# Kernel optimization log

Hardware: AMD Instinct MI355X
Metric: run time of the kernel (lower is better)

Reference implementation:

```python
import jax, jax.numpy as jnp
import numpy as np

N = 128       # n_channels
B = 131072    # batch
C = np.float32(np.sqrt(0.5))  # 50/50 beamsplitter amplitude (c = s = sqrt(0.5))


def setup_inputs() -> dict:
    key = jax.random.key(0)
    k1, k2, k3, k4 = jax.random.split(key, 4)
    M = N * (N - 1) // 2
    return {
        "x_real": jax.random.normal(k1, (B, N), jnp.float32),
        "x_imag": jax.random.normal(k2, (B, N), jnp.float32),
        "mzi_phases": jax.random.normal(k3, (M * 2,), jnp.float32) * 0.1,
        "output_phases": jax.random.normal(k4, (N,), jnp.float32) * 0.1,
    }


def _construct_unitary(mzi_phases, output_phases):
    n = output_phases.shape[0]
    m = n * (n - 1) // 2
    # pair ordering matches the torch double loop: i ascending, then j > i (row-major triu)
    i_np, j_np = np.triu_indices(n, 1)
    i_idx = jnp.asarray(i_np, jnp.int32)
    j_idx = jnp.asarray(j_np, jnp.int32)
    ph = mzi_phases.reshape(m, 2)
    theta, phi = ph[:, 0], ph[:, 1]

    def step(U, xs):
        th, ph_, i, j = xs
        e_phi = jax.lax.complex(jnp.cos(ph_), jnp.sin(ph_))
        e_th = jax.lax.complex(jnp.cos(th), jnp.sin(th))
        ri = U[i]
        rj = U[j]
        # T_ij @ U touches only rows i and j (O(N) Givens row update)
        new_i = C * ri + (C * e_phi) * rj
        new_j = (C * e_th) * ri - (C * e_th * e_phi) * rj
        U = U.at[i].set(new_i).at[j].set(new_j)
        return U, None

    def chunk_body(U, xs_chunk):
        U, _ = jax.lax.scan(step, U, xs_chunk)
        return U, None

    # chunk the M sequential updates: M = (n-1) * (n//2) for even n;
    # checkpointing chunks keeps reverse-mode memory O(sqrt-ish) instead of O(M * N^2)
    n_chunks = n - 1
    cs = n // 2
    xs = (theta.reshape(n_chunks, cs), phi.reshape(n_chunks, cs),
          i_idx.reshape(n_chunks, cs), j_idx.reshape(n_chunks, cs))
    U0 = jnp.eye(n, dtype=jnp.complex64)
    U, _ = jax.lax.scan(jax.checkpoint(chunk_body), U0, xs)
    # output phase screen D @ U
    d = jax.lax.complex(jnp.cos(output_phases), jnp.sin(output_phases))
    return d[:, None] * U


def reference(x_real, x_imag, mzi_phases, output_phases):
    U = _construct_unitary(mzi_phases, output_phases)           # [N, N] complex64
    x = jax.lax.complex(x_real, x_imag)                          # [B, N] complex64
    # matmul(U, x.unsqueeze(-1)).squeeze(-1) == x @ U^T
    out = jnp.einsum('nm,bm->bn', U, x)                          # [B, N] complex64
    # ComplexDropout is identity in eval mode
    return out
```

## Files before the change

kernel.cpp:

```cpp
#include <hip/hip_runtime.h>
#include <hip/hip_bf16.h>

#define NDIM 128
#define N2   (NDIM * NDIM)
#define BDIM 131072
#define NMZI 8128
#define NCHUNK 8
#define NBLK 32
#define NJG 8
#define NCOL 32
#define NLOC 16
static constexpr float CC = 0.70710678118654752440f;

typedef __attribute__((ext_vector_type(8))) short bf16x8;
typedef __attribute__((ext_vector_type(4))) float f32x4;

__device__ __align__(16) float2         g_V[NCHUNK * N2];
__device__ __align__(16) float2         g_W[4 * N2];
__device__ __align__(16) float2         g_Y[2 * N2];
__device__ __align__(16) unsigned short g_TB[32 * NDIM * 8];
__device__ __align__(16) unsigned short g_Ur[16 * NDIM * 8];
__device__ __align__(16) unsigned short g_Ui[16 * NDIM * 8];
__device__ unsigned g_ctr[3];

__device__ inline unsigned short f2bf(float f) {
    union { __hip_bfloat16 h; unsigned short u; } cv;
    cv.h = __float2bfloat16(f);
    return cv.u;
}

__device__ __forceinline__ void gbar(int idx) {
    __syncthreads();
    asm volatile("" ::: "memory");
    if (threadIdx.x == 0) {
        __threadfence();
        __hip_atomic_fetch_add(&g_ctr[idx], 1u, __ATOMIC_ACQ_REL, __HIP_MEMORY_SCOPE_AGENT);
        while (__hip_atomic_load(&g_ctr[idx], __ATOMIC_ACQUIRE, __HIP_MEMORY_SCOPE_AGENT)
               < (unsigned)NBLK)
            __builtin_amdgcn_s_sleep(8);
        __threadfence();
    }
    __syncthreads();
    asm volatile("" ::: "memory");
}

#define CFMA(acc, av, b)                                                    \
    acc.x = fmaf(av.x, b.x, fmaf(-av.y, b.y, acc.x));                       \
    acc.y = fmaf(av.x, b.y, fmaf( av.y, b.x, acc.y));

template <int MODE>
__device__ __forceinline__ void compose_unit(const float2* __restrict__ A,
                                             const float2* __restrict__ B,
                                             float2* __restrict__ Cout,
                                             const float* __restrict__ oph,
                                             int n0, int m, float2* __restrict__ As,
                                             bool active) {
    __syncthreads();
    if (active) {
        #pragma unroll
        for (int r = 0; r < 4; ++r) As[r * NDIM + m] = A[(n0 + r) * NDIM + m];
    }
    __syncthreads();
    if (!active) return;

    float2 a0 = {0.f, 0.f}, a1 = {0.f, 0.f}, a2 = {0.f, 0.f}, a3 = {0.f, 0.f};
    float2 bb[8];
    #pragma unroll
    for (int u = 0; u < 8; ++u) bb[u] = B[u * NDIM + m];

    #pragma unroll 1
    for (int k0 = 0; k0 < NDIM; k0 += 8) {
        #pragma unroll
        for (int u = 0; u < 8; ++u) {
            const float2 b = bb[u];
            bb[u] = B[(k0 + 8 + u) * NDIM + m];
            const int k = k0 + u;
            float2 v;
            v = As[0 * NDIM + k]; CFMA(a0, v, b)
            v = As[1 * NDIM + k]; CFMA(a1, v, b)
            v = As[2 * NDIM + k]; CFMA(a2, v, b)
            v = As[3 * NDIM + k]; CFMA(a3, v, b)
        }
    }
    if (MODE == 0) {
        Cout[(n0 + 0) * NDIM + m] = a0;
        Cout[(n0 + 1) * NDIM + m] = a1;
        Cout[(n0 + 2) * NDIM + m] = a2;
        Cout[(n0 + 3) * NDIM + m] = a3;
    } else {
        const int kg = m >> 3, e = m & 7;
        #pragma unroll
        for (int r = 0; r < 4; ++r) {
            const int n = n0 + r;
            const float2 u = (r == 0) ? a0 : (r == 1) ? a1 : (r == 2) ? a2 : a3;
            float ds, dc;
            sincosf(oph[n], &ds, &dc);
            const float vr = fmaf(u.x, dc, -u.y * ds);
            const float vi = fmaf(u.x, ds,  u.y * dc);
            g_TB[(kg * NDIM + n) * 8 + e]        = f2bf(vr);
            g_TB[((16 + kg) * NDIM + n) * 8 + e] = f2bf(-vi);
            g_Ur[(kg * NDIM + n) * 8 + e] = f2bf(vr);
            g_Ui[(kg * NDIM + n) * 8 + e] = f2bf(vi);
        }
    }
}

__global__ __launch_bounds__(256) void build_all(const float* __restrict__ mzi,
                                                 const float* __restrict__ oph) {
    __shared__ __align__(16) char SM[40960];
    const int tid = threadIdx.x;
    const int b   = blockIdx.x;

    {
        float2 (*Usm)[NCOL] = reinterpret_cast<float2(*)[NCOL]>(SM);
        float4 (*ph)[NDIM]  = reinterpret_cast<float4(*)[NDIM]>(SM + 32768);
        float4 (*cmp)[NCOL] = reinterpret_cast<float4(*)[NCOL]>(SM + 36864);
        const int c     = tid & 31;
        const int g     = tid >> 5;
        const int col0  = (b & 3) * NCOL;
        const int chunk = b >> 2;
        const int i0    = chunk * 16;

        for (int k = g; k < NDIM; k += NJG)
            Usm[k][c] = make_float2((k == col0 + c) ? 1.f : 0.f, 0.f);

        const float2* mzp = (const float2*)mzi;
        int base = 127 * i0 - (i0 * (i0 - 1)) / 2;
        {
            const int L0 = NDIM - 1 - i0;
            if (tid < L0) {
                const float2 mz = mzp[base + tid];
                float sp, cp, st, ct;
                sincosf(mz.y, &sp, &cp);
                sincosf(mz.x, &st, &ct);
                ph[0][tid] = make_float4(cp, sp, CC * ct, CC * st);
            }
        }
        __syncthreads();

        #pragma unroll 1
        for (int sw = 0; sw < 16; ++sw) {
            const int i = i0 + sw;
            const int L = NDIM - 1 - i;
            if (L <= 0) break;
            const int cur = sw & 1;

            float2 mznext;
            const bool have = (sw < 15) && (tid < L - 1);
            if (have) mznext = mzp[base + L + tid];

            const float2 r0 = Usm[i][c];
            const int nloc  = (L + NJG - 1) >> 3;
            const int myBeg = g * nloc;
            const int myN   = max(0, min(nloc, L - myBeg));

            float2 treg[NLOC];
            float2 qth[NLOC];
            float  A = 1.f;
            float2 Bc = make_float2(0.f, 0.f);
            #pragma unroll
            for (int kk = 0; kk < NLOC; ++kk) {
                if (kk < myN) {
                    const int off = myBeg + kk;
                    const float4 q  = ph[cur][off];
                    const float2 rj = Usm[i + 1 + off][c];
                    const float tr = fmaf(q.x, rj.x, -q.y * rj.y);
                    const float ti = fmaf(q.x, rj.y,  q.y * rj.x);
                    treg[kk] = make_float2(tr, ti);
                    qth[kk]  = make_float2(q.z, q.w);
                    Bc.x = CC * (Bc.x + tr);
                    Bc.y = CC * (Bc.y + ti);
                    A *= CC;
                }
            }
            cmp[g][c] = make_float4(A, Bc.x, Bc.y, 0.f);
            __syncthreads();

            float2 r = r0;
            for (int h2 = 0; h2 < g; ++h2) {
                const float4 cm = cmp[h2][c];
                r.x = fmaf(cm.x, r.x, cm.y);
                r.y = fmaf(cm.x, r.y, cm.z);
            }

            #pragma unroll
            for (int kk = 0; kk < NLOC; ++kk) {
                if (kk < myN) {
                    const float2 t = treg[kk];
                    const float2 q = qth[kk];
                    const float dr = r.x - t.x, di = r.y - t.y;
                    const float njx = fmaf(q.x, dr, -q.y * di);
                    const float njy = fmaf(q.x, di,  q.y * dr);
                    Usm[i + 1 + myBeg + kk][c] = make_float2(njx, njy);
                    r.x = CC * (r.x + t.x);
                    r.y = CC * (r.y + t.y);
                }
            }
            if (myN > 0 && (myBeg + myN == L))
                Usm[i][c] = r;

            if (have) {
                float sp, cp, st, ct;
                sincosf(mznext.y, &sp, &cp);
                sincosf(mznext.x, &st, &ct);
                ph[cur ^ 1][tid] = make_float4(cp, sp, CC * ct, CC * st);
            }
            __syncthreads();
            base += L;
        }

        float2* Vp = g_V + chunk * N2;
        for (int k = g; k < NDIM; k += NJG)
            Vp[k * NDIM + col0 + c] = Usm[k][c];
    }

    gbar(0);

    const int h = tid >> 7;
    const int m = tid & 127;
    float2* As = (float2*)(SM + h * 4096);

    #pragma unroll 1
    for (int pass = 0; pass < 2; ++pass) {
        const int u  = pass * 64 + 2 * b + h;
        const int p  = u >> 5;
        const int n0 = (u & 31) * 4;
        compose_unit<0>(g_V + (2 * p + 1) * N2, g_V + (2 * p) * N2,
                        g_W + p * N2, nullptr, n0, m, As, true);
    }

    gbar(1);

    {
        const int u  = 2 * b + h;
        const int p  = u >> 5;
        const int n0 = (u & 31) * 4;
        compose_unit<0>(g_W + (2 * p + 1) * N2, g_W + (2 * p) * N2,
                        g_Y + p * N2, nullptr, n0, m, As, true);
    }

    gbar(2);

    compose_unit<1>(g_Y + N2, g_Y, nullptr, oph, b * 4, m, As, h == 0);
}

__global__ __launch_bounds__(256) void cmatmul0(const float* __restrict__ xr,
                                                const float* __restrict__ xi,
                                                float* __restrict__ out) {
    if (blockIdx.x == 0 && threadIdx.x == 0) {
        g_ctr[0] = 0; g_ctr[1] = 0; g_ctr[2] = 0;
    }
    __shared__ __align__(16) char smX[4][8192];
    const int tid  = threadIdx.x;
    const int lane = tid & 63;
    const int w    = tid >> 6;
    const int r15  = lane & 15;
    const int kg4  = lane >> 4;
    const int l31  = lane & 31;
    const int lh   = lane >> 5;
    const int R    = blockIdx.x * 64 + w * 16;

    const f32x4* sre = (const f32x4*)(xr + (size_t)R * NDIM);
    const f32x4* sim = (const f32x4*)(xi + (size_t)R * NDIM);
    f32x4 G[16];
    #pragma unroll
    for (int p = 0; p < 8; ++p) G[p]     = __builtin_nontemporal_load(sre + p * 64 + lane);
    #pragma unroll
    for (int p = 0; p < 8; ++p) G[8 + p] = __builtin_nontemporal_load(sim + p * 64 + lane);

    char* buf = &smX[w][0];
    #pragma unroll
    for (int p = 0; p < 8; ++p) {
        const int row = 2 * p + lh;
        const int swz = (row & 7) << 4;
        uint2 v;
        v.x = ((unsigned)f2bf(G[p][1]) << 16) | f2bf(G[p][0]);
        v.y = ((unsigned)f2bf(G[p][3]) << 16) | f2bf(G[p][2]);
        *(uint2*)(buf + row * 512 + ((l31 * 8) ^ swz)) = v;
        v.x = ((unsigned)f2bf(G[8 + p][1]) << 16) | f2bf(G[8 + p][0]);
        v.y = ((unsigned)f2bf(G[8 + p][3]) << 16) | f2bf(G[8 + p][2]);
        *(uint2*)(buf + row * 512 + 256 + ((l31 * 8) ^ swz)) = v;
    }

    bf16x8 fx[8];
    const int rswz = (r15 & 7) << 4;
    #pragma unroll
    for (int kc = 0; kc < 8; ++kc) {
        const int off = (((kc & 3) * 64 + kg4 * 16) ^ rswz) + ((kc >= 4) ? 256 : 0);
        fx[kc] = *(const bf16x8*)(buf + r15 * 512 + off);
    }

    const bf16x8* gT = (const bf16x8*)g_TB;
    #pragma unroll
    for (int nt = 0; nt < 8; ++nt) {
        f32x4 a0 = {0.f, 0.f, 0.f, 0.f};
        f32x4 a1 = {0.f, 0.f, 0.f, 0.f};
        #pragma unroll
        for (int kc = 0; kc < 4; ++kc)
            a0 = __builtin_amdgcn_mfma_f32_16x16x32_bf16(
                gT[(kc * 4 + kg4) * NDIM + nt * 16 + r15], fx[kc], a0, 0, 0, 0);
        #pragma unroll
        for (int kc = 4; kc < 8; ++kc)
            a1 = __builtin_amdgcn_mfma_f32_16x16x32_bf16(
                gT[(kc * 4 + kg4) * NDIM + nt * 16 + r15], fx[kc], a1, 0, 0, 0);
        const f32x4 s = a0 + a1;
        *(f32x4*)(buf + r15 * 512 + ((nt * 64 + kg4 * 16) ^ rswz)) = s;
    }

    char* outp = (char*)(out + (size_t)R * NDIM);
    #pragma unroll
    for (int p = 0; p < 8; ++p) {
        const int bofs = p * 1024 + lane * 16;
        const int row  = bofs >> 9;
        const int colb = bofs & 511;
        const f32x4 v = *(const f32x4*)(buf + row * 512 + (colb ^ ((row & 7) << 4)));
        __builtin_nontemporal_store(v, (f32x4*)(outp + bofs));
    }
}

__global__ __launch_bounds__(256) void cmatmul1(const float* __restrict__ xr,
                                                const float* __restrict__ xi,
                                                ushort2* __restrict__ outp) {
    if (blockIdx.x == 0 && threadIdx.x == 0) {
        g_ctr[0] = 0; g_ctr[1] = 0; g_ctr[2] = 0;
    }
    const int lane  = threadIdx.x & 63;
    const int w     = threadIdx.x >> 6;
    const int btile = blockIdx.x * 64 + w * 16;
    const int r15   = lane & 15;
    const int kg4   = lane >> 4;
    const int bload = btile + r15;

    const bf16x8* Ur = (const bf16x8*)g_Ur;
    const bf16x8* Ui = (const bf16x8*)g_Ui;
    const float* xrp = xr + (size_t)bload * NDIM;
    const float* xip = xi + (size_t)bload * NDIM;

    bf16x8 ar[4], ai[4], ain[4];
    #pragma unroll
    for (int kc = 0; kc < 4; ++kc) {
        const int k0 = kc * 32 + kg4 * 8;
        float4 rlo = *(const float4*)(xrp + k0);
        float4 rhi = *(const float4*)(xrp + k0 + 4);
        float4 ilo = *(const float4*)(xip + k0);
        float4 ihi = *(const float4*)(xip + k0 + 4);
        bf16x8 vr, vi, vn;
        vr[0] = (short)f2bf(rlo.x); vr[1] = (short)f2bf(rlo.y);
        vr[2] = (short)f2bf(rlo.z); vr[3] = (short)f2bf(rlo.w);
        vr[4] = (short)f2bf(rhi.x); vr[5] = (short)f2bf(rhi.y);
        vr[6] = (short)f2bf(rhi.z); vr[7] = (short)f2bf(rhi.w);
        vi[0] = (short)f2bf(ilo.x); vi[1] = (short)f2bf(ilo.y);
        vi[2] = (short)f2bf(ilo.z); vi[3] = (short)f2bf(ilo.w);
        vi[4] = (short)f2bf(ihi.x); vi[5] = (short)f2bf(ihi.y);
        vi[6] = (short)f2bf(ihi.z); vi[7] = (short)f2bf(ihi.w);
        #pragma unroll
        for (int e = 0; e < 8; ++e) vn[e] = (short)(vi[e] ^ 0x8000);
        ar[kc] = vr; ai[kc] = vi; ain[kc] = vn;
    }

    #pragma unroll
    for (int nt = 0; nt < 8; ++nt) {
        f32x4 accR = {0.f, 0.f, 0.f, 0.f};
        f32x4 accI = {0.f, 0.f, 0.f, 0.f};
        #pragma unroll
        for (int kc = 0; kc < 4; ++kc) {
            const int kg = kc * 4 + kg4;
            bf16x8 br = Ur[kg * NDIM + nt * 16 + r15];
            bf16x8 bi = Ui[kg * NDIM + nt * 16 + r15];
            accR = __builtin_amdgcn_mfma_f32_16x16x32_bf16(ar[kc],  br, accR, 0, 0, 0);
            accR = __builtin_amdgcn_mfma_f32_16x16x32_bf16(ain[kc], bi, accR, 0, 0, 0);
            accI = __builtin_amdgcn_mfma_f32_16x16x32_bf16(ar[kc],  bi, accI, 0, 0, 0);
            accI = __builtin_amdgcn_mfma_f32_16x16x32_bf16(ai[kc],  br, accI, 0, 0, 0);
        }
        const int n    = nt * 16 + r15;
        const int brow = btile + kg4 * 4;
        #pragma unroll
        for (int r = 0; r < 4; ++r)
            outp[(size_t)(brow + r) * NDIM + n] = make_ushort2(f2bf(accR[r]), f2bf(accI[r]));
    }
}

extern "C" void kernel_launch(void* const* d_in, const int* in_sizes, int n_in,
                              void* d_out, int out_size, void* d_ws, size_t ws_size,
                              hipStream_t stream) {
    const float* xr  = (const float*)d_in[0];
    const float* xi  = (const float*)d_in[1];
    const float* mzi = (const float*)d_in[2];
    const float* oph = (const float*)d_in[3];

    build_all<<<dim3(NBLK), dim3(256), 0, stream>>>(mzi, oph);
    if (out_size == BDIM * NDIM) {
        cmatmul0<<<dim3(BDIM / 64), dim3(256), 0, stream>>>(xr, xi, (float*)d_out);
    } else {
        cmatmul1<<<dim3(BDIM / 64), dim3(256), 0, stream>>>(xr, xi, (ushort2*)d_out);
    }
}
```

Baseline: 130.6 us.

## Split unitary build into two chunks with a single compose and barrier

The sequential Givens sweep is now split into two uneven chunks at row 56, processed by 8 blocks, in place of 8 chunks of 16 rows. A single 2-way product then replaces the three-level tree of compositions, and two of the three grid barriers are gone. The barrier also uses relaxed polling and a shorter sleep. This removes barrier and composition overhead, but each active block now runs a much longer serial sweep (about 56-71 rows) and most blocks sit idle.

```diff
diff --git a/kernel.cpp b/kernel.cpp
--- a/kernel.cpp
+++ b/kernel.cpp
@@ -5,8 +5,8 @@
 #define N2   (NDIM * NDIM)
 #define BDIM 131072
 #define NMZI 8128
-#define NCHUNK 8
 #define NBLK 32
+#define SPLIT 56
 #define NJG 8
 #define NCOL 32
 #define NLOC 16
@@ -15,9 +15,7 @@
 typedef __attribute__((ext_vector_type(8))) short bf16x8;
 typedef __attribute__((ext_vector_type(4))) float f32x4;
 
-__device__ __align__(16) float2         g_V[NCHUNK * N2];
-__device__ __align__(16) float2         g_W[4 * N2];
-__device__ __align__(16) float2         g_Y[2 * N2];
+__device__ __align__(16) float2         g_V[2 * N2];
 __device__ __align__(16) unsigned short g_TB[32 * NDIM * 8];
 __device__ __align__(16) unsigned short g_Ur[16 * NDIM * 8];
 __device__ __align__(16) unsigned short g_Ui[16 * NDIM * 8];
@@ -29,15 +27,15 @@
     return cv.u;
 }
 
-__device__ __forceinline__ void gbar(int idx) {
+__device__ __forceinline__ void gbar0() {
     __syncthreads();
     asm volatile("" ::: "memory");
     if (threadIdx.x == 0) {
         __threadfence();
-        __hip_atomic_fetch_add(&g_ctr[idx], 1u, __ATOMIC_ACQ_REL, __HIP_MEMORY_SCOPE_AGENT);
-        while (__hip_atomic_load(&g_ctr[idx], __ATOMIC_ACQUIRE, __HIP_MEMORY_SCOPE_AGENT)
+        __hip_atomic_fetch_add(&g_ctr[0], 1u, __ATOMIC_RELEASE, __HIP_MEMORY_SCOPE_AGENT);
+        while (__hip_atomic_load(&g_ctr[0], __ATOMIC_RELAXED, __HIP_MEMORY_SCOPE_AGENT)
                < (unsigned)NBLK)
-            __builtin_amdgcn_s_sleep(8);
+            __builtin_amdgcn_s_sleep(2);
         __threadfence();
     }
     __syncthreads();
@@ -47,63 +45,6 @@
 #define CFMA(acc, av, b)                                                    \
     acc.x = fmaf(av.x, b.x, fmaf(-av.y, b.y, acc.x));                       \
     acc.y = fmaf(av.x, b.y, fmaf( av.y, b.x, acc.y));
-
-template <int MODE>
-__device__ __forceinline__ void compose_unit(const float2* __restrict__ A,
-                                             const float2* __restrict__ B,
-                                             float2* __restrict__ Cout,
-                                             const float* __restrict__ oph,
-                                             int n0, int m, float2* __restrict__ As,
-                                             bool active) {
-    __syncthreads();
-    if (active) {
-        #pragma unroll
-        for (int r = 0; r < 4; ++r) As[r * NDIM + m] = A[(n0 + r) * NDIM + m];
-    }
-    __syncthreads();
-    if (!active) return;
-
-    float2 a0 = {0.f, 0.f}, a1 = {0.f, 0.f}, a2 = {0.f, 0.f}, a3 = {0.f, 0.f};
-    float2 bb[8];
-    #pragma unroll
-    for (int u = 0; u < 8; ++u) bb[u] = B[u * NDIM + m];
-
-    #pragma unroll 1
-    for (int k0 = 0; k0 < NDIM; k0 += 8) {
-        #pragma unroll
-        for (int u = 0; u < 8; ++u) {
-            const float2 b = bb[u];
-            bb[u] = B[(k0 + 8 + u) * NDIM + m];
-            const int k = k0 + u;
-            float2 v;
-            v = As[0 * NDIM + k]; CFMA(a0, v, b)
-            v = As[1 * NDIM + k]; CFMA(a1, v, b)
-            v = As[2 * NDIM + k]; CFMA(a2, v, b)
-            v = As[3 * NDIM + k]; CFMA(a3, v, b)
-        }
-    }
-    if (MODE == 0) {
-        Cout[(n0 + 0) * NDIM + m] = a0;
-        Cout[(n0 + 1) * NDIM + m] = a1;
-        Cout[(n0 + 2) * NDIM + m] = a2;
-        Cout[(n0 + 3) * NDIM + m] = a3;
-    } else {
-        const int kg = m >> 3, e = m & 7;
-        #pragma unroll
-        for (int r = 0; r < 4; ++r) {
-            const int n = n0 + r;
-            const float2 u = (r == 0) ? a0 : (r == 1) ? a1 : (r == 2) ? a2 : a3;
-            float ds, dc;
-            sincosf(oph[n], &ds, &dc);
-            const float vr = fmaf(u.x, dc, -u.y * ds);
-            const float vi = fmaf(u.x, ds,  u.y * dc);
-            g_TB[(kg * NDIM + n) * 8 + e]        = f2bf(vr);
-            g_TB[((16 + kg) * NDIM + n) * 8 + e] = f2bf(-vi);
-            g_Ur[(kg * NDIM + n) * 8 + e] = f2bf(vr);
-            g_Ui[(kg * NDIM + n) * 8 + e] = f2bf(vi);
-        }
-    }
-}
 
 __global__ __launch_bounds__(256) void build_all(const float* __restrict__ mzi,
                                                  const float* __restrict__ oph) {
@@ -111,7 +52,7 @@
     const int tid = threadIdx.x;
     const int b   = blockIdx.x;
 
-    {
+    if (b < 8) {
         float2 (*Usm)[NCOL] = reinterpret_cast<float2(*)[NCOL]>(SM);
         float4 (*ph)[NDIM]  = reinterpret_cast<float4(*)[NDIM]>(SM + 32768);
         float4 (*cmp)[NCOL] = reinterpret_cast<float4(*)[NCOL]>(SM + 36864);
@@ -119,7 +60,9 @@
         const int g     = tid >> 5;
         const int col0  = (b & 3) * NCOL;
         const int chunk = b >> 2;
-        const int i0    = chunk * 16;
+        const int i0    = chunk ? SPLIT : 0;
+        const int iEnd  = chunk ? (NDIM - 1) : SPLIT;
+        const int nsw   = iEnd - i0;
 
         for (int k = g; k < NDIM; k += NJG)
             Usm[k][c] = make_float2((k == col0 + c) ? 1.f : 0.f, 0.f);
@@ -139,14 +82,13 @@
         __syncthreads();
 
         #pragma unroll 1
-        for (int sw = 0; sw < 16; ++sw) {
+        for (int sw = 0; sw < nsw; ++sw) {
             const int i = i0 + sw;
             const int L = NDIM - 1 - i;
-            if (L <= 0) break;
             const int cur = sw & 1;
 
             float2 mznext;
-            const bool have = (sw < 15) && (tid < L - 1);
+            const bool have = (sw < nsw - 1) && (tid < L - 1);
             if (have) mznext = mzp[base + L + tid];
 
             const float2 r0 = Usm[i][c];
@@ -214,41 +156,67 @@
             Vp[k * NDIM + col0 + c] = Usm[k][c];
     }
 
-    gbar(0);
-
-    const int h = tid >> 7;
-    const int m = tid & 127;
-    float2* As = (float2*)(SM + h * 4096);
-
-    #pragma unroll 1
-    for (int pass = 0; pass < 2; ++pass) {
-        const int u  = pass * 64 + 2 * b + h;
-        const int p  = u >> 5;
-        const int n0 = (u & 31) * 4;
-        compose_unit<0>(g_V + (2 * p + 1) * N2, g_V + (2 * p) * N2,
-                        g_W + p * N2, nullptr, n0, m, As, true);
-    }
-
-    gbar(1);
+    gbar0();
 
     {
-        const int u  = 2 * b + h;
-        const int p  = u >> 5;
-        const int n0 = (u & 31) * 4;
-        compose_unit<0>(g_W + (2 * p + 1) * N2, g_W + (2 * p) * N2,
-                        g_Y + p * N2, nullptr, n0, m, As, true);
-    }
-
-    gbar(2);
-
-    compose_unit<1>(g_Y + N2, g_Y, nullptr, oph, b * 4, m, As, h == 0);
+        const int h  = tid >> 7;
+        const int m  = tid & 127;
+        const int n0 = b * 4;
+        float2* As = (float2*)SM;
+        const float2* A = g_V + N2;
+        const float2* B = g_V;
+
+        __syncthreads();
+        if (h == 0) {
+            #pragma unroll
+            for (int r = 0; r < 4; ++r) As[r * NDIM + m] = A[(n0 + r) * NDIM + m];
+        }
+        __syncthreads();
+        if (h == 0) {
+            float2 a0 = {0.f, 0.f}, a1 = {0.f, 0.f}, a2 = {0.f, 0.f}, a3 = {0.f, 0.f};
+            float2 bb[8];
+            #pragma unroll
+            for (int u = 0; u < 8; ++u) bb[u] = B[u * NDIM + m];
+
+            #pragma unroll 1
+            for (int k0 = 0; k0 < NDIM; k0 += 8) {
+                #pragma unroll
+                for (int u = 0; u < 8; ++u) {
+                    const float2 bv = bb[u];
+                    bb[u] = B[(k0 + 8 + u) * NDIM + m];
+                    const int k = k0 + u;
+                    float2 v;
+                    v = As[0 * NDIM + k]; CFMA(a0, v, bv)
+                    v = As[1 * NDIM + k]; CFMA(a1, v, bv)
+                    v = As[2 * NDIM + k]; CFMA(a2, v, bv)
+                    v = As[3 * NDIM + k]; CFMA(a3, v, bv)
+                }
+            }
+            const int kg = m >> 3, e = m & 7;
+            #pragma unroll
+            for (int r = 0; r < 4; ++r) {
+                const int n = n0 + r;
+                const float2 u = (r == 0) ? a0 : (r == 1) ? a1 : (r == 2) ? a2 : a3;
+                float ds, dc;
+                sincosf(oph[n], &ds, &dc);
+                const float vr = fmaf(u.x, dc, -u.y * ds);
+                const float vi = fmaf(u.x, ds,  u.y * dc);
+                g_TB[(kg * NDIM + n) * 8 + e]        = f2bf(vr);
+                g_TB[((16 + kg) * NDIM + n) * 8 + e] = f2bf(-vi);
+                g_Ur[(kg * NDIM + n) * 8 + e] = f2bf(vr);
+                g_Ui[(kg * NDIM + n) * 8 + e] = f2bf(vi);
+            }
+        }
+    }
 }
 
 __global__ __launch_bounds__(256) void cmatmul0(const float* __restrict__ xr,
                                                 const float* __restrict__ xi,
                                                 float* __restrict__ out) {
     if (blockIdx.x == 0 && threadIdx.x == 0) {
-        g_ctr[0] = 0; g_ctr[1] = 0; g_ctr[2] = 0;
+        #pragma unroll
+        for (int i = 0; i < 3; ++i)
+            __hip_atomic_store(&g_ctr[i], 0u, __ATOMIC_RELAXED, __HIP_MEMORY_SCOPE_AGENT);
     }
     __shared__ __align__(16) char smX[4][8192];
     const int tid  = threadIdx.x;
@@ -322,7 +290,9 @@
                                                 const float* __restrict__ xi,
                                                 ushort2* __restrict__ outp) {
     if (blockIdx.x == 0 && threadIdx.x == 0) {
-        g_ctr[0] = 0; g_ctr[1] = 0; g_ctr[2] = 0;
+        #pragma unroll
+        for (int i = 0; i < 3; ++i)
+            __hip_atomic_store(&g_ctr[i], 0u, __ATOMIC_RELAXED, __HIP_MEMORY_SCOPE_AGENT);
     }
     const int lane  = threadIdx.x & 63;
     const int w     = threadIdx.x >> 6;
```

Result: slower. 169.0 us (+29.4%).
